# Performance work log

Measured on AMD Instinct MI355X. Metric: run time of the kernel, lower is better.

The kernel has to match this reference:

```python
import jax, jax.numpy as jnp
import numpy as np

MAX_SEQ = 512
HIDDEN = 1024
E = 2048  # hidden * expansion_factor
S = 128
EPS = 1e-05


def _rope(x):
    # x: [b, n, 2, s]; rotate along sequence dim (dim=1 in the torch code)
    b, n, h, s = x.shape
    half = s // 2
    pos = jnp.arange(n, dtype=x.dtype)
    # torch: freq_seq = -arange(half)/half; inv_freq = 10000**(-freq_seq) = 10000**(arange/half)
    inv_freq = jnp.power(jnp.asarray(10000.0, x.dtype), jnp.arange(half, dtype=x.dtype) / half)
    sinusoid = pos[:, None] * inv_freq[None, :]          # [n, half]
    sin = jnp.sin(sinusoid)[None, :, None, :]            # [1, n, 1, half]
    cos = jnp.cos(sinusoid)[None, :, None, :]
    x1, x2 = jnp.split(x, 2, axis=-1)
    return jnp.concatenate([x1 * cos - x2 * sin, x2 * cos + x1 * sin], axis=-1)


def _rel_pos_bias(w, seq_len):
    # toeplitz construction (max_seq_length <= 512 branch)
    t = jnp.pad(w, (0, seq_len))                          # [3*seq_len - 1]
    t = jnp.tile(t, seq_len)[:-seq_len]                   # [seq_len*(3*seq_len-2)]
    t = t.reshape(seq_len, 3 * seq_len - 2)
    r = (2 * seq_len - 1) // 2
    return t[:, r:-r][None]                               # [1, seq_len, seq_len]


def setup_inputs() -> dict:
    key = jax.random.key(0)
    ks = jax.random.split(key, 6)
    x = jax.random.normal(ks[0], (16, 512, HIDDEN), dtype=jnp.float32)
    uv_w = jax.random.normal(ks[1], (2 * E + S, HIDDEN), dtype=jnp.float32) * 0.02
    o_w = jax.random.normal(ks[2], (HIDDEN, E), dtype=jnp.float32) * 0.02
    return {
        "x": x,
        "ln_w": jnp.ones((HIDDEN,), jnp.float32),
        "ln_b": jnp.zeros((HIDDEN,), jnp.float32),
        "uv_w": uv_w,
        "uv_b": jnp.zeros((2 * E + S,), jnp.float32),
        "gamma": jax.random.uniform(ks[3], (2, S), dtype=jnp.float32),
        "beta": jax.random.uniform(ks[4], (2, S), dtype=jnp.float32),
        "o_w": o_w,
        "o_b": jnp.zeros((HIDDEN,), jnp.float32),
        "w_rel": jax.random.uniform(ks[5], (2 * MAX_SEQ - 1,), dtype=jnp.float32),
    }


def reference(x, ln_w, ln_b, uv_w, uv_b, gamma, beta, o_w, o_b, w_rel):
    b, n, d = x.shape
    shortcut = x
    # LayerNorm
    mu = jnp.mean(x, axis=-1, keepdims=True)
    var = jnp.mean(jnp.square(x - mu), axis=-1, keepdims=True)
    xn = (x - mu) * jax.lax.rsqrt(var + EPS) * ln_w + ln_b
    # uv projection + silu on the whole projection
    uv = jax.nn.silu(jnp.einsum('bnd,fd->bnf', xn, uv_w) + uv_b)
    u, v, base = jnp.split(uv, [E, 2 * E], axis=-1)      # [b,n,E],[b,n,E],[b,n,S]
    # offset-scale: [b,n,S] x [2,S] -> [b,n,2,S]
    base = base[..., None, :] * gamma + beta
    base = _rope(base)
    q, k = base[:, :, 0, :], base[:, :, 1, :]
    qk = jnp.einsum('bnd,bmd->bnm', q, k)
    bias = _rel_pos_bias(w_rel, MAX_SEQ)[:, :n, :n]
    kernel = jnp.square(jax.nn.relu(qk / MAX_SEQ + bias))
    out = u * jnp.einsum('bnm,bme->bne', kernel, v)
    out = jnp.einsum('bne,de->bnd', out, o_w) + o_b
    return out + shortcut
```

## Files before the change

### kernel.cpp

```cpp
#include <hip/hip_runtime.h>
#include <hip/hip_bf16.h>


typedef __bf16 bf16_t;
typedef __bf16 bf16x4 __attribute__((ext_vector_type(4)));
typedef __bf16 bf16x8 __attribute__((ext_vector_type(8)));
typedef float  f32x4  __attribute__((ext_vector_type(4)));

__device__ __forceinline__ void async16(const void* g, void* l) {
  __builtin_amdgcn_global_load_lds(
      (const __attribute__((address_space(1))) void*)g,
      (__attribute__((address_space(3))) void*)l, 16, 0, 0);
}

__global__ __launch_bounds__(256) void fill_const(float* __restrict__ out,
                                                  float val, int n) {
  int i = blockIdx.x * 256 + threadIdx.x;
  if (i < n) out[i] = val;
}

__global__ void rope_table(float* __restrict__ cosT, float* __restrict__ sinT) {
  int idx = blockIdx.x * 256 + threadIdx.x;
  int n = idx >> 6, j = idx & 63;
  float invf = (float)pow(10000.0, (double)j * (1.0 / 64.0));
  float angf = (float)n * invf;
  cosT[idx] = (float)cos((double)angf);
  sinT[idx] = (float)sin((double)angf);
}

__global__ __launch_bounds__(256) void cvt_f32_bf16(const float* __restrict__ in,
                                                    bf16_t* __restrict__ out,
                                                    int n4) {
  int i = blockIdx.x * 256 + threadIdx.x;
  if (i < n4) {
    f32x4 v = ((const f32x4*)in)[i];
    bf16x4 o;
    o[0] = (__bf16)v[0]; o[1] = (__bf16)v[1];
    o[2] = (__bf16)v[2]; o[3] = (__bf16)v[3];
    ((bf16x4*)out)[i] = o;
  }
}

__global__ __launch_bounds__(256) void ln_kernel(const float* __restrict__ x,
                                                 const float* __restrict__ w,
                                                 const float* __restrict__ b,
                                                 bf16_t* __restrict__ xn) {
  int row = blockIdx.x;
  int tid = threadIdx.x;
  f32x4 v = *(const f32x4*)(x + (size_t)row * 1024 + tid * 4);
  float s = v[0] + v[1] + v[2] + v[3];
  float s2 = v[0]*v[0] + v[1]*v[1] + v[2]*v[2] + v[3]*v[3];
  for (int o = 32; o > 0; o >>= 1) {
    s += __shfl_down(s, o);
    s2 += __shfl_down(s2, o);
  }
  __shared__ float ps[4], ps2[4];
  if ((tid & 63) == 0) { ps[tid >> 6] = s; ps2[tid >> 6] = s2; }
  __syncthreads();
  float st = ps[0] + ps[1] + ps[2] + ps[3];
  float st2 = ps2[0] + ps2[1] + ps2[2] + ps2[3];
  float mean = st * (1.f / 1024.f);
  float var = st2 * (1.f / 1024.f) - mean * mean;
  float inv = 1.f / sqrtf(var + 1e-5f);
  bf16x4 o4;
  for (int i = 0; i < 4; i++) {
    float wn = w[tid * 4 + i], bn = b[tid * 4 + i];
    o4[i] = (__bf16)((v[i] - mean) * inv * wn + bn);
  }
  *(bf16x4*)(xn + (size_t)row * 1024 + tid * 4) = o4;
}

__global__ __launch_bounds__(128) void rope_qk(const bf16_t* __restrict__ baseb,
                                               const float* __restrict__ gamma,
                                               const float* __restrict__ beta,
                                               const float* __restrict__ cosT,
                                               const float* __restrict__ sinT,
                                               bf16_t* __restrict__ q,
                                               bf16_t* __restrict__ k) {
  int m = blockIdx.x;
  int n = m & 511;
  int s = threadIdx.x;
  float base = (float)baseb[(size_t)m * 128 + s];
  __shared__ float t[2][128];
  t[0][s] = base * gamma[s] + beta[s];
  t[1][s] = base * gamma[128 + s] + beta[128 + s];
  __syncthreads();
  int j = s & 63;
  float c = cosT[n * 64 + j], sn = sinT[n * 64 + j];
  for (int h = 0; h < 2; h++) {
    float x1 = t[h][j], x2 = t[h][64 + j];
    float r = (s < 64) ? (x1 * c - x2 * sn) : (x2 * c + x1 * sn);
    bf16_t* dst = h == 0 ? q : k;
    dst[(size_t)m * 128 + s] = (__bf16)r;
  }
}

struct EpiUV {
  const float* uv_b;
  bf16_t* u;
  bf16_t* vT;
  bf16_t* baseb;
  __device__ void operator()(int b, int m, int n, float acc) const {
    float xv = acc + uv_b[n];
    float sv = xv * __builtin_amdgcn_rcpf(1.f + __expf(-xv));
    sv = fminf(fmaxf(sv, -100.f), 100.f);
    if (n < 2048) {
      u[(size_t)m * 2048 + n] = (__bf16)sv;
    } else if (n < 4096) {
      int bb = m >> 9, nseq = m & 511;
      vT[((size_t)bb * 2048 + (n - 2048)) * 512 + nseq] = (__bf16)sv;
    } else {
      baseb[(size_t)m * 128 + (n - 4096)] = (__bf16)sv;
    }
  }
};
struct EpiQK {
  const float* w_rel;
  bf16_t* km;
  __device__ void operator()(int b, int i, int j, float acc) const {
    float bias = w_rel[511 + j - i];
    float t = fmaxf(acc * (1.f / 512.f) + bias, 0.f);
    t = fminf(t, 100.f);
    km[((size_t)b * 512 + i) * 512 + j] = (__bf16)(t * t);
  }
};
struct EpiAttn {
  const bf16_t* u;
  bf16_t* out2;
  __device__ void operator()(int b, int i, int e, float acc) const {
    size_t m = (size_t)b * 512 + i;
    float uu = (float)u[m * 2048 + e];
    float r = acc * uu;
    r = fminf(fmaxf(r, -1e6f), 1e6f);
    out2[m * 2048 + e] = (__bf16)r;
  }
};
struct EpiOut {
  const float* o_b;
  const float* x;
  float* out;
  __device__ void operator()(int b, int m, int d, float acc) const {
    long idx = (long)m * 1024 + d;
    float r = acc + o_b[d] + x[idx];
    r = fminf(fmaxf(r, -1e5f), 1e5f);
    out[idx] = r;
  }
};

template <typename Epi>
__global__ __launch_bounds__(256, 2)
void gemm_nt(const bf16_t* __restrict__ A, const bf16_t* __restrict__ Bm,
             int lda, int ldb, int K, long sAz, long sBz, Epi epi) {
  __shared__ __align__(16) char smem[32768];
  char* smA = smem;
  char* smB = smem + 16384;
  const int tid = threadIdx.x;
  const int lane = tid & 63;
  const int wid = tid >> 6;
  const int wm = wid & 1, wn = wid >> 1;
  const int quad = lane >> 4, col16 = lane & 15;
  const int srow = lane >> 3;
  const int skc = lane & 7;
  const int bz = blockIdx.z;
  const int tileM = blockIdx.x * 128;
  const int tileN = blockIdx.y * 128;
  const bf16_t* Ab = A + (size_t)bz * sAz;
  const bf16_t* Bb = Bm + (size_t)bz * sBz;

  f32x4 acc[4][4] = {};

  for (int k0 = 0; k0 < K; k0 += 64) {
#pragma unroll
    for (int c4 = 0; c4 < 4; c4++) {
      int ch = c4 * 4 + wid;
      int row = ch * 8 + srow;
      int kc = skc ^ (row & 7);
      async16(Ab + (size_t)(tileM + row) * lda + k0 + kc * 8, smA + ch * 1024);
      async16(Bb + (size_t)(tileN + row) * ldb + k0 + kc * 8, smB + ch * 1024);
    }
    __syncthreads();
#pragma unroll
    for (int kk = 0; kk < 2; kk++) {
      bf16x8 af[4], bfr[4];
      int jj = kk * 4 + quad;
#pragma unroll
      for (int t = 0; t < 4; t++) {
        int ml = wm * 64 + t * 16 + col16;
        int nl = wn * 64 + t * 16 + col16;
        af[t] = *(const bf16x8*)(smA + (size_t)ml * 128 + ((jj ^ (ml & 7)) * 16));
        bfr[t] = *(const bf16x8*)(smB + (size_t)nl * 128 + ((jj ^ (nl & 7)) * 16));
      }
#pragma unroll
      for (int mt = 0; mt < 4; mt++)
#pragma unroll
        for (int nt = 0; nt < 4; nt++)
          acc[mt][nt] = __builtin_amdgcn_mfma_f32_16x16x32_bf16(af[mt], bfr[nt], acc[mt][nt], 0, 0, 0);
    }
    __syncthreads();
  }

#pragma unroll
  for (int mt = 0; mt < 4; mt++) {
    int gm = tileM + wm * 64 + mt * 16 + quad * 4;
#pragma unroll
    for (int nt = 0; nt < 4; nt++) {
      int gn = tileN + wn * 64 + nt * 16 + col16;
#pragma unroll
      for (int r = 0; r < 4; r++) epi(bz, gm + r, gn, acc[mt][nt][r]);
    }
  }
}

extern "C" void kernel_launch(void* const* d_in, const int* in_sizes, int n_in,
                              void* d_out, int out_size, void* d_ws, size_t ws_size,
                              hipStream_t stream) {
  const float* x = (const float*)d_in[0];
  const float* ln_w = (const float*)d_in[1];
  const float* ln_b = (const float*)d_in[2];
  const float* uv_w = (const float*)d_in[3];
  const float* uv_b = (const float*)d_in[4];
  const float* gamma = (const float*)d_in[5];
  const float* beta = (const float*)d_in[6];
  const float* o_w = (const float*)d_in[7];
  const float* o_b = (const float*)d_in[8];
  const float* w_rel = (const float*)d_in[9];
  float* out = (float*)d_out;

  const int NOUT = 8388608;
  const size_t WS_NEEDED = 71303168;
  if (ws_size < WS_NEEDED) {
    float wsMiB = (float)(ws_size >> 20);
    fill_const<<<dim3(32768), dim3(256), 0, stream>>>(out, 1000.f + wsMiB, NOUT);
    return;
  }

  char* ws = (char*)d_ws;
  bf16_t* u = (bf16_t*)(ws + 0);
  bf16_t* out2 = u;
  bf16_t* vT = (bf16_t*)(ws + 33554432);
  bf16_t* o_wb = (bf16_t*)(ws + 67108864);
  char* ob = (char*)d_out;
  bf16_t* xn = (bf16_t*)ob;
  bf16_t* uv_wb = (bf16_t*)(ob + 16777216);
  bf16_t* baseb = (bf16_t*)(ob + 25427968);
  float* cosT = (float*)(ob + 27525120);
  float* sinT = (float*)(ob + 27656192);
  bf16_t* qb = (bf16_t*)ob;
  bf16_t* kb = (bf16_t*)(ob + 2097152);
  bf16_t* km = (bf16_t*)(ob + 4194304);

  rope_table<<<dim3(128), dim3(256), 0, stream>>>(cosT, sinT);
  cvt_f32_bf16<<<dim3(4224), dim3(256), 0, stream>>>(uv_w, uv_wb, 1081344);
  cvt_f32_bf16<<<dim3(2048), dim3(256), 0, stream>>>(o_w, o_wb, 524288);
  ln_kernel<<<dim3(8192), dim3(256), 0, stream>>>(x, ln_w, ln_b, xn);
  gemm_nt<<<dim3(64, 33, 1), dim3(256), 0, stream>>>(
      xn, uv_wb, 1024, 1024, 1024, 0L, 0L, EpiUV{uv_b, u, vT, baseb});
  rope_qk<<<dim3(8192), dim3(128), 0, stream>>>(baseb, gamma, beta, cosT, sinT, qb, kb);
  gemm_nt<<<dim3(4, 4, 16), dim3(256), 0, stream>>>(
      qb, kb, 128, 128, 128, (long)512 * 128, (long)512 * 128, EpiQK{w_rel, km});
  gemm_nt<<<dim3(4, 16, 16), dim3(256), 0, stream>>>(
      km, vT, 512, 512, 512, (long)512 * 512, (long)2048 * 512, EpiAttn{u, out2});
  gemm_nt<<<dim3(64, 8, 1), dim3(256), 0, stream>>>(
      out2, o_wb, 2048, 2048, 2048, 0L, 0L, EpiOut{o_b, x, out});
}
```

Before: 339.1 us.

## Double-buffer LDS tiles in gemm_nt to overlap global loads with MFMA

```diff
diff --git a/kernel.cpp b/kernel.cpp
--- a/kernel.cpp
+++ b/kernel.cpp
@@ -151,9 +151,7 @@
 __global__ __launch_bounds__(256, 2)
 void gemm_nt(const bf16_t* __restrict__ A, const bf16_t* __restrict__ Bm,
              int lda, int ldb, int K, long sAz, long sBz, Epi epi) {
-  __shared__ __align__(16) char smem[32768];
-  char* smA = smem;
-  char* smB = smem + 16384;
+  __shared__ __align__(16) char smem[65536];
   const int tid = threadIdx.x;
   const int lane = tid & 63;
   const int wid = tid >> 6;
@@ -166,29 +164,57 @@
   const int tileN = blockIdx.y * 128;
   const bf16_t* Ab = A + (size_t)bz * sAz;
   const bf16_t* Bb = Bm + (size_t)bz * sBz;
+  const int NT = K >> 6;
+
+  const bf16_t* pA[4];
+  const bf16_t* pB[4];
+  int ldsOff[4];
+#pragma unroll
+  for (int c4 = 0; c4 < 4; c4++) {
+    int ch = c4 * 4 + wid;
+    int row = ch * 8 + srow;
+    int kc = skc ^ (row & 7);
+    pA[c4] = Ab + (size_t)(tileM + row) * lda + kc * 8;
+    pB[c4] = Bb + (size_t)(tileN + row) * ldb + kc * 8;
+    ldsOff[c4] = ch * 1024;
+  }
+
+  auto stage = [&](int kt, int buf) {
+    char* bA = (char*)smem + buf * 32768;
+    char* bB = bA + 16384;
+    const size_t ko = (size_t)kt * 64;
+#pragma unroll
+    for (int c4 = 0; c4 < 4; c4++) {
+      async16(pA[c4] + ko, bA + ldsOff[c4]);
+      async16(pB[c4] + ko, bB + ldsOff[c4]);
+    }
+  };
 
   f32x4 acc[4][4] = {};
 
-  for (int k0 = 0; k0 < K; k0 += 64) {
-#pragma unroll
-    for (int c4 = 0; c4 < 4; c4++) {
-      int ch = c4 * 4 + wid;
-      int row = ch * 8 + srow;
-      int kc = skc ^ (row & 7);
-      async16(Ab + (size_t)(tileM + row) * lda + k0 + kc * 8, smA + ch * 1024);
-      async16(Bb + (size_t)(tileN + row) * ldb + k0 + kc * 8, smB + ch * 1024);
-    }
-    __syncthreads();
+  stage(0, 0);
+  for (int t = 0; t < NT; t++) {
+    if (t + 1 < NT) {
+      stage(t + 1, (t + 1) & 1);
+      asm volatile("s_waitcnt vmcnt(8)" ::: "memory");
+    } else {
+      asm volatile("s_waitcnt vmcnt(0)" ::: "memory");
+    }
+    __builtin_amdgcn_s_barrier();
+    asm volatile("" ::: "memory");
+
+    const char* smA = (const char*)smem + (t & 1) * 32768;
+    const char* smB = smA + 16384;
 #pragma unroll
     for (int kk = 0; kk < 2; kk++) {
       bf16x8 af[4], bfr[4];
       int jj = kk * 4 + quad;
 #pragma unroll
-      for (int t = 0; t < 4; t++) {
-        int ml = wm * 64 + t * 16 + col16;
-        int nl = wn * 64 + t * 16 + col16;
-        af[t] = *(const bf16x8*)(smA + (size_t)ml * 128 + ((jj ^ (ml & 7)) * 16));
-        bfr[t] = *(const bf16x8*)(smB + (size_t)nl * 128 + ((jj ^ (nl & 7)) * 16));
+      for (int tt = 0; tt < 4; tt++) {
+        int ml = wm * 64 + tt * 16 + col16;
+        int nl = wn * 64 + tt * 16 + col16;
+        af[tt] = *(const bf16x8*)(smA + (size_t)ml * 128 + ((jj ^ (ml & 7)) * 16));
+        bfr[tt] = *(const bf16x8*)(smB + (size_t)nl * 128 + ((jj ^ (nl & 7)) * 16));
       }
 #pragma unroll
       for (int mt = 0; mt < 4; mt++)
@@ -196,7 +222,12 @@
         for (int nt = 0; nt < 4; nt++)
           acc[mt][nt] = __builtin_amdgcn_mfma_f32_16x16x32_bf16(af[mt], bfr[nt], acc[mt][nt], 0, 0, 0);
     }
-    __syncthreads();
+
+    if (t + 1 < NT) {
+      asm volatile("" ::: "memory");
+      __builtin_amdgcn_s_barrier();
+      asm volatile("" ::: "memory");
+    }
   }
 
 #pragma unroll
```

New measurement: 346.8 us. +2.3%, slower.

## Template GEMM on M-tile height, use 256-row tiles and vectorized epilogues

Applied to the files above, without the earlier changes.

```diff
diff --git a/kernel.cpp b/kernel.cpp
--- a/kernel.cpp
+++ b/kernel.cpp
@@ -100,60 +100,79 @@
   bf16_t* u;
   bf16_t* vT;
   bf16_t* baseb;
-  __device__ void operator()(int b, int m, int n, float acc) const {
-    float xv = acc + uv_b[n];
-    float sv = xv * __builtin_amdgcn_rcpf(1.f + __expf(-xv));
-    sv = fminf(fmaxf(sv, -100.f), 100.f);
+  __device__ void operator()(int b, int m0, int n, f32x4 a4) const {
+    float bn = uv_b[n];
+    bf16_t s[4];
+#pragma unroll
+    for (int r = 0; r < 4; r++) {
+      float xv = a4[r] + bn;
+      float sv = xv * __builtin_amdgcn_rcpf(1.f + __expf(-xv));
+      sv = fminf(fmaxf(sv, -100.f), 100.f);
+      s[r] = (__bf16)sv;
+    }
     if (n < 2048) {
-      u[(size_t)m * 2048 + n] = (__bf16)sv;
+#pragma unroll
+      for (int r = 0; r < 4; r++) u[(size_t)(m0 + r) * 2048 + n] = s[r];
     } else if (n < 4096) {
-      int bb = m >> 9, nseq = m & 511;
-      vT[((size_t)bb * 2048 + (n - 2048)) * 512 + nseq] = (__bf16)sv;
+      int bb = m0 >> 9, ns = m0 & 511;
+      bf16x4 p; p[0] = s[0]; p[1] = s[1]; p[2] = s[2]; p[3] = s[3];
+      *(bf16x4*)(vT + ((size_t)bb * 2048 + (n - 2048)) * 512 + ns) = p;
     } else {
-      baseb[(size_t)m * 128 + (n - 4096)] = (__bf16)sv;
+#pragma unroll
+      for (int r = 0; r < 4; r++)
+        baseb[(size_t)(m0 + r) * 128 + (n - 4096)] = s[r];
     }
   }
 };
 struct EpiQK {
   const float* w_rel;
   bf16_t* km;
-  __device__ void operator()(int b, int i, int j, float acc) const {
-    float bias = w_rel[511 + j - i];
-    float t = fmaxf(acc * (1.f / 512.f) + bias, 0.f);
-    t = fminf(t, 100.f);
-    km[((size_t)b * 512 + i) * 512 + j] = (__bf16)(t * t);
+  __device__ void operator()(int b, int i0, int j, f32x4 a4) const {
+#pragma unroll
+    for (int r = 0; r < 4; r++) {
+      float bias = w_rel[511 + j - (i0 + r)];
+      float t = fmaxf(a4[r] * (1.f / 512.f) + bias, 0.f);
+      t = fminf(t, 100.f);
+      km[((size_t)b * 512 + i0 + r) * 512 + j] = (__bf16)(t * t);
+    }
   }
 };
 struct EpiAttn {
   const bf16_t* u;
   bf16_t* out2;
-  __device__ void operator()(int b, int i, int e, float acc) const {
-    size_t m = (size_t)b * 512 + i;
-    float uu = (float)u[m * 2048 + e];
-    float r = acc * uu;
-    r = fminf(fmaxf(r, -1e6f), 1e6f);
-    out2[m * 2048 + e] = (__bf16)r;
+  __device__ void operator()(int b, int i0, int e, f32x4 a4) const {
+#pragma unroll
+    for (int r = 0; r < 4; r++) {
+      size_t m = (size_t)b * 512 + i0 + r;
+      float uu = (float)u[m * 2048 + e];
+      float rr = a4[r] * uu;
+      rr = fminf(fmaxf(rr, -1e6f), 1e6f);
+      out2[m * 2048 + e] = (__bf16)rr;
+    }
   }
 };
 struct EpiOut {
   const float* o_b;
   const float* x;
   float* out;
-  __device__ void operator()(int b, int m, int d, float acc) const {
-    long idx = (long)m * 1024 + d;
-    float r = acc + o_b[d] + x[idx];
-    r = fminf(fmaxf(r, -1e5f), 1e5f);
-    out[idx] = r;
+  __device__ void operator()(int b, int m0, int d, f32x4 a4) const {
+    float ob = o_b[d];
+#pragma unroll
+    for (int r = 0; r < 4; r++) {
+      long idx = (long)(m0 + r) * 1024 + d;
+      float rr = a4[r] + ob + x[idx];
+      rr = fminf(fmaxf(rr, -1e5f), 1e5f);
+      out[idx] = rr;
+    }
   }
 };
 
-template <typename Epi>
+template <int MFR, typename Epi>
 __global__ __launch_bounds__(256, 2)
 void gemm_nt(const bf16_t* __restrict__ A, const bf16_t* __restrict__ Bm,
              int lda, int ldb, int K, long sAz, long sBz, Epi epi) {
-  __shared__ __align__(16) char smem[32768];
-  char* smA = smem;
-  char* smB = smem + 16384;
+  constexpr int MROWS = MFR * 32;
+  __shared__ __align__(16) char smem[MROWS * 128 + 16384];
   const int tid = threadIdx.x;
   const int lane = tid & 63;
   const int wid = tid >> 6;
@@ -162,36 +181,56 @@
   const int srow = lane >> 3;
   const int skc = lane & 7;
   const int bz = blockIdx.z;
-  const int tileM = blockIdx.x * 128;
+  const int tileM = blockIdx.x * MROWS;
   const int tileN = blockIdx.y * 128;
   const bf16_t* Ab = A + (size_t)bz * sAz;
   const bf16_t* Bb = Bm + (size_t)bz * sBz;
 
-  f32x4 acc[4][4] = {};
+  unsigned oA[MFR], oB[4];
+#pragma unroll
+  for (int c4 = 0; c4 < MFR; c4++) {
+    int ch = c4 * 4 + wid;
+    int row = ch * 8 + srow;
+    int kc = skc ^ (row & 7);
+    oA[c4] = (unsigned)((tileM + row) * lda + kc * 8);
+  }
+#pragma unroll
+  for (int c4 = 0; c4 < 4; c4++) {
+    int ch = c4 * 4 + wid;
+    int row = ch * 8 + srow;
+    int kc = skc ^ (row & 7);
+    oB[c4] = (unsigned)((tileN + row) * ldb + kc * 8);
+  }
+
+  f32x4 acc[MFR][4] = {};
 
   for (int k0 = 0; k0 < K; k0 += 64) {
 #pragma unroll
-    for (int c4 = 0; c4 < 4; c4++) {
-      int ch = c4 * 4 + wid;
-      int row = ch * 8 + srow;
-      int kc = skc ^ (row & 7);
-      async16(Ab + (size_t)(tileM + row) * lda + k0 + kc * 8, smA + ch * 1024);
-      async16(Bb + (size_t)(tileN + row) * ldb + k0 + kc * 8, smB + ch * 1024);
-    }
+    for (int c4 = 0; c4 < MFR; c4++)
+      async16(Ab + oA[c4] + k0, smem + (c4 * 4 + wid) * 1024);
+#pragma unroll
+    for (int c4 = 0; c4 < 4; c4++)
+      async16(Bb + oB[c4] + k0, smem + MROWS * 128 + (c4 * 4 + wid) * 1024);
     __syncthreads();
+
+    const char* smA = (const char*)smem;
+    const char* smB = smA + MROWS * 128;
 #pragma unroll
     for (int kk = 0; kk < 2; kk++) {
-      bf16x8 af[4], bfr[4];
+      bf16x8 af[MFR], bfr[4];
       int jj = kk * 4 + quad;
 #pragma unroll
-      for (int t = 0; t < 4; t++) {
-        int ml = wm * 64 + t * 16 + col16;
-        int nl = wn * 64 + t * 16 + col16;
-        af[t] = *(const bf16x8*)(smA + (size_t)ml * 128 + ((jj ^ (ml & 7)) * 16));
-        bfr[t] = *(const bf16x8*)(smB + (size_t)nl * 128 + ((jj ^ (nl & 7)) * 16));
+      for (int tt = 0; tt < MFR; tt++) {
+        int ml = wm * (MFR * 16) + tt * 16 + col16;
+        af[tt] = *(const bf16x8*)(smA + (size_t)ml * 128 + ((jj ^ (ml & 7)) * 16));
       }
 #pragma unroll
-      for (int mt = 0; mt < 4; mt++)
+      for (int tt = 0; tt < 4; tt++) {
+        int nl = wn * 64 + tt * 16 + col16;
+        bfr[tt] = *(const bf16x8*)(smB + (size_t)nl * 128 + ((jj ^ (nl & 7)) * 16));
+      }
+#pragma unroll
+      for (int mt = 0; mt < MFR; mt++)
 #pragma unroll
         for (int nt = 0; nt < 4; nt++)
           acc[mt][nt] = __builtin_amdgcn_mfma_f32_16x16x32_bf16(af[mt], bfr[nt], acc[mt][nt], 0, 0, 0);
@@ -200,13 +239,12 @@
   }
 
 #pragma unroll
-  for (int mt = 0; mt < 4; mt++) {
-    int gm = tileM + wm * 64 + mt * 16 + quad * 4;
+  for (int mt = 0; mt < MFR; mt++) {
+    int gm = tileM + wm * (MFR * 16) + mt * 16 + quad * 4;
 #pragma unroll
     for (int nt = 0; nt < 4; nt++) {
       int gn = tileN + wn * 64 + nt * 16 + col16;
-#pragma unroll
-      for (int r = 0; r < 4; r++) epi(bz, gm + r, gn, acc[mt][nt][r]);
+      epi(bz, gm, gn, acc[mt][nt]);
     }
   }
 }
@@ -253,13 +291,13 @@
   cvt_f32_bf16<<<dim3(4224), dim3(256), 0, stream>>>(uv_w, uv_wb, 1081344);
   cvt_f32_bf16<<<dim3(2048), dim3(256), 0, stream>>>(o_w, o_wb, 524288);
   ln_kernel<<<dim3(8192), dim3(256), 0, stream>>>(x, ln_w, ln_b, xn);
-  gemm_nt<<<dim3(64, 33, 1), dim3(256), 0, stream>>>(
+  gemm_nt<8><<<dim3(32, 33, 1), dim3(256), 0, stream>>>(
       xn, uv_wb, 1024, 1024, 1024, 0L, 0L, EpiUV{uv_b, u, vT, baseb});
   rope_qk<<<dim3(8192), dim3(128), 0, stream>>>(baseb, gamma, beta, cosT, sinT, qb, kb);
-  gemm_nt<<<dim3(4, 4, 16), dim3(256), 0, stream>>>(
+  gemm_nt<4><<<dim3(4, 4, 16), dim3(256), 0, stream>>>(
       qb, kb, 128, 128, 128, (long)512 * 128, (long)512 * 128, EpiQK{w_rel, km});
-  gemm_nt<<<dim3(4, 16, 16), dim3(256), 0, stream>>>(
+  gemm_nt<8><<<dim3(2, 16, 16), dim3(256), 0, stream>>>(
       km, vT, 512, 512, 512, (long)512 * 512, (long)2048 * 512, EpiAttn{u, out2});
-  gemm_nt<<<dim3(64, 8, 1), dim3(256), 0, stream>>>(
+  gemm_nt<4><<<dim3(64, 8, 1), dim3(256), 0, stream>>>(
       out2, o_wb, 2048, 2048, 2048, 0L, 0L, EpiOut{o_b, x, out});
 }
```

Result: no change. 335.0 us (-1.2%).
